# Kernel tuning notes

Measured on AMD Instinct MI355X. Metric: run time of the kernel, lower is better.

Reference implementation:

```python
import jax, jax.numpy as jnp
import numpy as np

B, N, K, D, H = 1, 2048, 32, 128, 8
DH = D // H
EPS = 1e-5


def eq_linear(s, v, Ws, bs, Wv):
    # scalar channels: affine; vector channels: linear only (equivariance)
    return s @ Ws + bs, jnp.einsum('...ix,io->...ox', v, Wv)


def dtp(s1, v1, s2, v2, w=None):
    # depthwise tensor product paths: s*s, v.v (scalars); s1*v2, s2*v1 (vectors)
    ss = s1 * s2
    vv = jnp.sum(v1 * v2, axis=-1)
    sv = s1[..., None] * v2
    vs = s2[..., None] * v1
    if w is not None:  # w: [4, ...] per-path per-channel weights
        ss = ss * w[0]
        vv = vv * w[1]
        sv = sv * w[2][..., None]
        vs = vs * w[3][..., None]
    return jnp.concatenate([ss, vv], -1), jnp.concatenate([sv, vs], -2)


def eq_layer_norm(s, v, gs, bs, gv):
    mu = s.mean(-1, keepdims=True)
    var = ((s - mu) ** 2).mean(-1, keepdims=True)
    s_ln = (s - mu) / jnp.sqrt(var + EPS) * gs + bs
    # vectors: normalize by RMS of channel norms (rotation-equivariant)
    rms = jnp.sqrt(jnp.mean(jnp.sum(v * v, -1), -1, keepdims=True) + EPS)
    v_ln = v / rms[..., None] * gv[..., None]
    return s_ln, v_ln


def layer_norm(x, g, b):
    mu = x.mean(-1, keepdims=True)
    var = ((x - mu) ** 2).mean(-1, keepdims=True)
    return (x - mu) / jnp.sqrt(var + EPS) * g + b


def setup_inputs() -> dict:
    key = jax.random.key(0)
    ks = jax.random.split(key, 32)
    r = lambda i, sh, sc=1.0: jax.random.normal(ks[i], sh, jnp.float32) * sc
    inp = {
        'query_s': r(0, (B, N, D)), 'query_v': r(1, (B, N, D, 3)),
        'key_s': r(2, (B, N, D)), 'key_v': r(3, (B, N, D, 3)),
        'edge_irrep_s': r(4, (B, N, K)), 'edge_irrep_v': r(5, (B, N, K, 3)),
        'edge_emb': r(6, (B, N, K, D)),
        'pair_attn_mask': jnp.logical_or(
            jax.random.randint(ks[7], (B, N, K), 0, 2) > 0, jnp.arange(K) == 0),
        'knn_key_index': jax.random.randint(ks[8], (B, N, K), 0, N),
        # EquivariantLinear params
        'Wq_s': r(9, (D, D), D ** -0.5), 'Wq_v': r(10, (D, D), D ** -0.5), 'bq': jnp.zeros(D),
        'Wk_s': r(11, (D, D), D ** -0.5), 'Wk_v': r(12, (D, D), D ** -0.5), 'bk': jnp.zeros(D),
        'Wqk_s': r(13, (2 * DH, DH), (2 * DH) ** -0.5), 'Wqk_v': r(14, (2 * DH, DH), (2 * DH) ** -0.5), 'bqk': jnp.zeros(DH),
        'Wdtp': r(15, (D, 4 * D), D ** -0.5), 'bdtp': jnp.zeros(4 * D),
        'Wagv_s': r(16, (H, 2 * DH, 3 * DH), (2 * DH) ** -0.5), 'bagv': jnp.zeros((H, 3 * DH)),
        'Wagv_v': r(17, (H, 2 * DH, DH), (2 * DH) ** -0.5),
        'Wattn': r(18, (DH,), DH ** -0.5),
        'Wval_s': r(19, (2 * DH, DH), (2 * DH) ** -0.5), 'Wval_v': r(20, (2 * DH, DH), (2 * DH) ** -0.5), 'bval': jnp.zeros(DH),
        'Wo_s': r(21, (D, D), D ** -0.5), 'Wo_v': r(22, (D, D), D ** -0.5), 'bo': jnp.zeros(D),
        'ln_gs': jnp.ones(D), 'ln_bs': jnp.zeros(D), 'ln_gv': jnp.ones(D),
        'lna_g': jnp.ones(DH), 'lna_b': jnp.zeros(DH),
    }
    return inp


def reference(query_s, query_v, key_s, key_v, edge_irrep_s, edge_irrep_v, edge_emb,
              pair_attn_mask, knn_key_index,
              Wq_s, Wq_v, bq, Wk_s, Wk_v, bk, Wqk_s, Wqk_v, bqk, Wdtp, bdtp,
              Wagv_s, bagv, Wagv_v, Wattn, Wval_s, Wval_v, bval, Wo_s, Wo_v, bo,
              ln_gs, ln_bs, ln_gv, lna_g, lna_b):
    # pre-LN + skip (LAYER_NORM_ON_SKIP=True: skip taken after LN)
    qs, qv = eq_layer_norm(query_s, query_v, ln_gs, ln_bs, ln_gv)
    skip_s, skip_v = qs, qv
    qs, qv = eq_linear(qs, qv, Wq_s, bq, Wq_v)
    ksc, kvc = eq_linear(key_s, key_v, Wk_s, bk, Wk_v)
    # KNN gather of keys per query: [B,Q,K,D] / [B,Q,K,D,3]
    bidx = jnp.arange(B)[:, None, None]
    ks_g = ksc[bidx, knn_key_index]
    kv_g = kvc[bidx, knn_key_index]
    # depthwise tensor product query x gathered keys -> [B,Q,K,2D]
    qk_s, qk_v = dtp(qs[:, :, None, :], qv[:, :, None, :, :], ks_g, kv_g)
    # split heads -> [H,B,Q,K,2DH]
    qk_s = jnp.moveaxis(qk_s.reshape(B, N, K, H, 2 * DH), -2, 0)
    qk_v = jnp.moveaxis(qk_v.reshape(B, N, K, H, 2 * DH, 3), -3, 0)
    qk_s, qk_v = eq_linear(qk_s, qk_v, Wqk_s, bqk, Wqk_v)  # [H,B,Q,K,DH]
    # edge-conditioned TP weights: [4,H,B,Q,K,DH]
    w = (edge_emb @ Wdtp + bdtp).reshape(B, N, K, 4, H, DH)
    w = jnp.transpose(w, (3, 4, 0, 1, 2, 5))
    e_s = edge_irrep_s[..., None]        # [B,Q,K,1]
    e_v = edge_irrep_v[..., None, :]     # [B,Q,K,1,3]
    qk_s, qk_v = dtp(qk_s, qk_v, e_s, e_v, w)  # [H,B,Q,K,2DH]
    # multi-head attn/gate/value projection
    agv = jnp.einsum('hbqki,hio->hbqko', qk_s, Wagv_s) + bagv[:, None, None, None, :]
    val_v = jnp.einsum('hbqkix,hio->hbqkox', qk_v, Wagv_v)  # [H,B,Q,K,DH,3]
    attn_feat, gate, val_s = jnp.split(agv, 3, axis=-1)
    attn = jnp.einsum('hbqkd,d->hbqk', layer_norm(attn_feat, lna_g, lna_b), Wattn)
    attn = jnp.where(pair_attn_mask[None], attn, jnp.finfo(attn.dtype).min)
    attn = jax.nn.softmax(attn, axis=-1)
    # gate activation: SiLU on scalars, sigmoid-gate on vectors
    val_s = jax.nn.silu(val_s)
    val_v = val_v * jax.nn.sigmoid(gate)[..., None]
    # value-edge tensor product + projection
    vs2, vv2 = dtp(val_s, val_v, e_s, e_v)
    vs2, vv2 = eq_linear(vs2, vv2, Wval_s, bval, Wval_v)  # [H,B,Q,K,DH]
    # attention-weighted aggregation over neighbors
    out_s = jnp.einsum('hbqkd,hbqk->hbqd', vs2, attn)
    out_v = jnp.einsum('hbqkdx,hbqk->hbqdx', vv2, attn)
    out_s = jnp.moveaxis(out_s, 0, -2).reshape(B, N, D)
    out_v = jnp.moveaxis(out_v, 0, -3).reshape(B, N, D, 3)
    out_s, out_v = eq_linear(out_s, out_v, Wo_s, bo, Wo_v)
    return out_s + skip_s, out_v + skip_v, attn
```

## Files before the change

### kernel.cpp

```cpp
#include <hip/hip_runtime.h>
#include <hip/hip_bf16.h>
#include <math.h>

#define N_Q 2048
#define K_E 32
#define D_F 128
#define H_N 8
#define DH_N 16
#define EPS_F 1e-5f
#define NEGMAX -3.4028235e38f
#define EPB 8


__global__ __launch_bounds__(64) void k_prep(
    const int* __restrict__ mask, int* __restrict__ kidx, int* __restrict__ ucnt,
    float* __restrict__ attn_raw, float* __restrict__ mbuf)
{
    const int n = blockIdx.x, t = threadIdx.x;
    const int k = t & 31;
    int mk = (t < 32) ? mask[n*K_E + k] : 0;
    unsigned long long bal = __ballot(mk != 0);
    int u = (int)__popcll(bal);
    if (t < 32 && mk) {
        int pos = (int)__popcll(bal & ((1ull << k) - 1ull));
        kidx[n*K_E + pos] = k;
    }
    if (t == 0) ucnt[n] = u;
    if (mask[n*K_E + k] == 0) {
        int hb = (t >> 5) * 4;
        #pragma unroll
        for (int hh = 0; hh < 4; ++hh)
            attn_raw[(size_t)(hb + hh)*(N_Q*K_E) + n*K_E + k] = NEGMAX;
    }
    int gU = (u + 7) >> 3;
    if (t < 16) {
        for (int g2 = gU; g2 < 4; ++g2)
            mbuf[(n*4 + g2)*16 + t] = (t < 8) ? NEGMAX : 0.f;
    }
}

__global__ __launch_bounds__(128) void k_qk(
    const float* __restrict__ qs_in, const float* __restrict__ qv_in,
    const float* __restrict__ ks_in, const float* __restrict__ kv_in,
    const float* __restrict__ Wq_s, const float* __restrict__ Wq_v, const float* __restrict__ bq,
    const float* __restrict__ Wk_s, const float* __restrict__ Wk_v, const float* __restrict__ bk,
    const float* __restrict__ ln_gs, const float* __restrict__ ln_bs, const float* __restrict__ ln_gv,
    float4* __restrict__ q4, float4* __restrict__ k4,
    float* __restrict__ skip_s, float* __restrict__ skip_v)
{
    const int t = threadIdx.x;
    __shared__ __align__(16) float raw[D_F*3];
    __shared__ float4 sv[D_F];
    __shared__ float red[6];
    if (blockIdx.x < N_Q) {
        const int n = blockIdx.x;
        float sval = qs_in[n*D_F + t];
        float ssqp = 0.f;
        if (t < 96) {
            float4 rv = ((const float4*)(qv_in + (size_t)n*D_F*3))[t];
            ((float4*)raw)[t] = rv;
            ssqp = rv.x*rv.x + rv.y*rv.y + rv.z*rv.z + rv.w*rv.w;
        }
        float r0 = sval, r1 = sval*sval, r2 = ssqp;
        #pragma unroll
        for (int m = 1; m < 64; m <<= 1) {
            r0 += __shfl_xor(r0, m);
            r1 += __shfl_xor(r1, m);
            r2 += __shfl_xor(r2, m);
        }
        if ((t & 63) == 0) { int w = t >> 6; red[w*3+0]=r0; red[w*3+1]=r1; red[w*3+2]=r2; }
        __syncthreads();
        float tS = red[0]+red[3], tS2 = red[1]+red[4], tQ = red[2]+red[5];
        float mu = tS * (1.f/D_F);
        float var = fmaxf(tS2*(1.f/D_F) - mu*mu, 0.f);
        float rstd = rsqrtf(var + EPS_F);
        float rrms = rsqrtf(tQ*(1.f/D_F) + EPS_F);
        float a = (sval - mu)*rstd*ln_gs[t] + ln_bs[t];
        skip_s[n*D_F + t] = a;
        float gv = ln_gv[t];
        float b0 = raw[t*3+0]*rrms*gv;
        float b1 = raw[t*3+1]*rrms*gv;
        float b2 = raw[t*3+2]*rrms*gv;
        skip_v[(n*D_F + t)*3 + 0] = b0;
        skip_v[(n*D_F + t)*3 + 1] = b1;
        skip_v[(n*D_F + t)*3 + 2] = b2;
        sv[t] = make_float4(b0, b1, b2, a);
        __syncthreads();
        float acc = bq[t], a0 = 0.f, a1 = 0.f, a2 = 0.f;
        #pragma unroll 4
        for (int i = 0; i < D_F; ++i) {
            float4 p = sv[i];
            float ws = Wq_s[i*D_F + t];
            float wv = Wq_v[i*D_F + t];
            acc += p.w*ws; a0 += p.x*wv; a1 += p.y*wv; a2 += p.z*wv;
        }
        q4[n*D_F + t] = make_float4(a0, a1, a2, acc);
    } else {
        const int n = blockIdx.x - N_Q;
        float sval = ks_in[n*D_F + t];
        if (t < 96) ((float4*)raw)[t] = ((const float4*)(kv_in + (size_t)n*D_F*3))[t];
        __syncthreads();
        sv[t] = make_float4(raw[t*3+0], raw[t*3+1], raw[t*3+2], sval);
        __syncthreads();
        float acc = bk[t], a0 = 0.f, a1 = 0.f, a2 = 0.f;
        #pragma unroll 4
        for (int i = 0; i < D_F; ++i) {
            float4 p = sv[i];
            float ws = Wk_s[i*D_F + t];
            float wv = Wk_v[i*D_F + t];
            acc += p.w*ws; a0 += p.x*wv; a1 += p.y*wv; a2 += p.z*wv;
        }
        k4[n*D_F + t] = make_float4(a0, a1, a2, acc);
    }
}

__global__ __launch_bounds__(512, 6) void k_edge_flash(
    const float4* __restrict__ q4, const float4* __restrict__ k4,
    const float* __restrict__ eis, const float* __restrict__ eiv,
    const float* __restrict__ eemb,
    const int* __restrict__ knn,
    const int* __restrict__ kidx, const int* __restrict__ ucnt,
    const float* __restrict__ Wqk_s, const float* __restrict__ Wqk_v, const float* __restrict__ bqk,
    const float* __restrict__ Wdtp, const float* __restrict__ bdtp,
    const float* __restrict__ Wagv_s, const float* __restrict__ bagv, const float* __restrict__ Wagv_v,
    const float* __restrict__ Wattn, const float* __restrict__ lna_g, const float* __restrict__ lna_b,
    const float* __restrict__ Wval_s, const float* __restrict__ Wval_v, const float* __restrict__ bval,
    float4* __restrict__ pbuf, float* __restrict__ mbuf, float* __restrict__ attn_raw)
{
    const int n = blockIdx.x & (N_Q - 1);
    const int g = blockIdx.x >> 11;
    const int base = n*K_E;
    const int u = ucnt[n];
    if ((g << 3) >= u) return;

    const int t = threadIdx.x;
    const int s = t >> 7, c = t & 127, h = (t >> 4) & 7, o = t & 15;
    const int rot2 = h * 2;

    __shared__ float4 ch[EPB*256];
    __shared__ float4 w4[EPB*128];
    __shared__ float  afeat[EPB*8*17];
    __shared__ float  mred[16];

    {
        float* ee = (float*)ch;
        {
            int idx = t; int m = idx & 7, i = idx >> 3;
            int jj = (g<<3) + m; jj = (jj < u) ? jj : (u-1);
            int e = base + kidx[base + jj];
            ee[i*EPB+m] = eemb[(size_t)e*D_F + i];
        }
        {
            int idx = t + 512; int m = idx & 7, i = idx >> 3;
            int jj = (g<<3) + m; jj = (jj < u) ? jj : (u-1);
            int e = base + kidx[base + jj];
            ee[i*EPB+m] = eemb[(size_t)e*D_F + i];
        }
        __syncthreads();
        float acc[EPB];
        float b = bdtp[t];
        #pragma unroll
        for (int m = 0; m < EPB; ++m) acc[m] = b;
        #pragma unroll 2
        for (int i = 0; i < D_F; ++i) {
            float wv = Wdtp[i*512 + t];
            #pragma unroll
            for (int m = 0; m < EPB; ++m) acc[m] += ee[i*EPB+m]*wv;
        }
        __syncthreads();
        float* w4f = (float*)w4;
        const int chn = t & 127, sel = t >> 7;
        #pragma unroll
        for (int m = 0; m < EPB; ++m)
            w4f[(m*128 + chn)*4 + sel] = acc[m];
    }

    const int mA = s, mB = s + 4;
    int jA = (g<<3) + mA; jA = (jA < u) ? jA : (u-1);
    int jB = (g<<3) + mB; jB = (jB < u) ? jB : (u-1);
    const int eA = base + kidx[base + jA];
    const int eB = base + kidx[base + jB];

    const float esA = eis[eA], esB = eis[eB];
    const float evAx = eiv[eA*3+0], evAy = eiv[eA*3+1], evAz = eiv[eA*3+2];
    const float evBx = eiv[eB*3+0], evBy = eiv[eB*3+1], evBz = eiv[eB*3+2];

    {
        float4 q  = q4[(size_t)n*D_F + c];
        float4 kA = k4[(size_t)knn[eA]*D_F + c];
        float4 kB = k4[(size_t)knn[eB]*D_F + c];
        const int hp = c >> 5, jc = c & 31;
        const int pos0 = hp*32 + ((jc + 2*hp) & 31);
        const int pos1 = (hp+4)*32 + ((jc + 2*(hp+4)) & 31);
        ch[mA*256 + pos0] = make_float4(q.w*kA.x, q.w*kA.y, q.w*kA.z, q.w*kA.w);
        ch[mA*256 + pos1] = make_float4(kA.w*q.x, kA.w*q.y, kA.w*q.z,
                                        q.x*kA.x + q.y*kA.y + q.z*kA.z);
        ch[mB*256 + pos0] = make_float4(q.w*kB.x, q.w*kB.y, q.w*kB.z, q.w*kB.w);
        ch[mB*256 + pos1] = make_float4(kB.w*q.x, kB.w*q.y, kB.w*q.z,
                                        q.x*kB.x + q.y*kB.y + q.z*kB.z);
    }
    __syncthreads();

    const int chA = mA*256 + h*32, chB = mB*256 + h*32;

    float pAs, pA0, pA1, pA2, pBs, pB0, pB1, pB2;
    {
        const float bqk_r = bqk[o];
        pAs = bqk_r; pA0 = 0.f; pA1 = 0.f; pA2 = 0.f;
        pBs = bqk_r; pB0 = 0.f; pB1 = 0.f; pB2 = 0.f;
        #pragma unroll 4
        for (int i = 0; i < 32; ++i) {
            int ph = (i + rot2) & 31;
            float4 cA = ch[chA + ph];
            float4 cB = ch[chB + ph];
            float ws = Wqk_s[i*16 + o];
            float wv = Wqk_v[i*16 + o];
            pAs += cA.w*ws; pA0 += cA.x*wv; pA1 += cA.y*wv; pA2 += cA.z*wv;
            pBs += cB.w*ws; pB0 += cB.x*wv; pB1 += cB.y*wv; pB2 += cB.z*wv;
        }
    }
    __syncthreads();

    const int posA = h*32 + ((o + rot2) & 31);
    const int posB = h*32 + ((o + 16 + rot2) & 31);

    {
        float4 wA = w4[mA*128 + c];
        float4 wB = w4[mB*128 + c];
        ch[mA*256 + posA] = make_float4(pAs*evAx*wA.z, pAs*evAy*wA.z, pAs*evAz*wA.z, pAs*esA*wA.x);
        float dA = pA0*evAx + pA1*evAy + pA2*evAz;
        ch[mA*256 + posB] = make_float4(esA*pA0*wA.w, esA*pA1*wA.w, esA*pA2*wA.w, dA*wA.y);
        ch[mB*256 + posA] = make_float4(pBs*evBx*wB.z, pBs*evBy*wB.z, pBs*evBz*wB.z, pBs*esB*wB.x);
        float dB = pB0*evBx + pB1*evBy + pB2*evBz;
        ch[mB*256 + posB] = make_float4(esB*pB0*wB.w, esB*pB1*wB.w, esB*pB2*wB.w, dB*wB.y);
    }
    __syncthreads();

    float gtA, vlA, vA0, vA1, vA2, gtB, vlB, vB0, vB1, vB2;
    {
        const float bag0 = bagv[h*48 + o];
        const float bag1 = bagv[h*48 + 16 + o];
        const float bag2 = bagv[h*48 + 32 + o];
        float atA = bag0, atB = bag0;
        gtA = bag1; vlA = bag2; vA0 = 0.f; vA1 = 0.f; vA2 = 0.f;
        gtB = bag1; vlB = bag2; vB0 = 0.f; vB1 = 0.f; vB2 = 0.f;
        #pragma unroll 4
        for (int i = 0; i < 32; ++i) {
            int ph = (i + rot2) & 31;
            float4 cA = ch[chA + ph];
            float4 cB = ch[chB + ph];
            const float* wrow = &Wagv_s[(h*32+i)*48];
            float w0 = wrow[o], w1 = wrow[16+o], w2 = wrow[32+o];
            float wv = Wagv_v[(h*32+i)*16 + o];
            atA += cA.w*w0; gtA += cA.w*w1; vlA += cA.w*w2;
            vA0 += cA.x*wv; vA1 += cA.y*wv; vA2 += cA.z*wv;
            atB += cB.w*w0; gtB += cB.w*w1; vlB += cB.w*w2;
            vB0 += cB.x*wv; vB1 += cB.y*wv; vB2 += cB.z*wv;
        }
        afeat[(mA*8 + h)*17 + o] = atA;
        afeat[(mB*8 + h)*17 + o] = atB;
    }
    __syncthreads();

    if (t < EPB*H_N) {
        int m2 = t >> 3, h2 = t & 7;
        const float* afr = &afeat[(m2*8 + h2)*17];
        float mu = 0.f;
        #pragma unroll 4
        for (int d2 = 0; d2 < DH_N; ++d2) mu += afr[d2];
        mu *= (1.f/DH_N);
        float var = 0.f;
        #pragma unroll 4
        for (int d2 = 0; d2 < DH_N; ++d2) { float dd = afr[d2]-mu; var += dd*dd; }
        var *= (1.f/DH_N);
        float rstd = rsqrtf(var + EPS_F);
        float logit = 0.f;
        #pragma unroll 4
        for (int d2 = 0; d2 < DH_N; ++d2) {
            float xn = (afr[d2]-mu)*rstd*lna_g[d2] + lna_b[d2];
            logit += xn*Wattn[d2];
        }
        int jj = (g<<3) + m2;
        bool vok = jj < u;
        if (vok) {
            int kor = kidx[base + jj];
            attn_raw[h2*(N_Q*K_E) + n*K_E + kor] = logit;
        } else {
            logit = NEGMAX;
        }
        afeat[(m2*8 + h2)*17 + 16] = logit;
        float mx = logit;
        mx = fmaxf(mx, __shfl_xor(mx, 8));
        mx = fmaxf(mx, __shfl_xor(mx, 16));
        mx = fmaxf(mx, __shfl_xor(mx, 32));
        float ex = expf(logit - mx);
        ex += __shfl_xor(ex, 8);
        ex += __shfl_xor(ex, 16);
        ex += __shfl_xor(ex, 32);
        if (m2 == 0) { mred[h2] = mx; mred[8 + h2] = ex; }
    }
    float sactA = vlA / (1.f + expf(-vlA));
    float gA = 1.f / (1.f + expf(-gtA));
    float qA0 = vA0*gA, qA1 = vA1*gA, qA2 = vA2*gA;
    float sactB = vlB / (1.f + expf(-vlB));
    float gB = 1.f / (1.f + expf(-gtB));
    float qB0 = vB0*gB, qB1 = vB1*gB, qB2 = vB2*gB;

    {
        ch[mA*256 + posA] = make_float4(sactA*evAx, sactA*evAy, sactA*evAz, sactA*esA);
        float dA = qA0*evAx + qA1*evAy + qA2*evAz;
        ch[mA*256 + posB] = make_float4(esA*qA0, esA*qA1, esA*qA2, dA);
        ch[mB*256 + posA] = make_float4(sactB*evBx, sactB*evBy, sactB*evBz, sactB*esB);
        float dB = qB0*evBx + qB1*evBy + qB2*evBz;
        ch[mB*256 + posB] = make_float4(esB*qB0, esB*qB1, esB*qB2, dB);
    }
    __syncthreads();

    {
        const float bval_r = bval[o];
        float vsA = bval_r, uA0 = 0.f, uA1 = 0.f, uA2 = 0.f;
        float vsB = bval_r, uB0 = 0.f, uB1 = 0.f, uB2 = 0.f;
        #pragma unroll 4
        for (int i = 0; i < 32; ++i) {
            int ph = (i + rot2) & 31;
            float4 cA = ch[chA + ph];
            float4 cB = ch[chB + ph];
            float ws = Wval_s[i*16 + o];
            float wv = Wval_v[i*16 + o];
            vsA += cA.w*ws; uA0 += cA.x*wv; uA1 += cA.y*wv; uA2 += cA.z*wv;
            vsB += cB.w*ws; uB0 += cB.x*wv; uB1 += cB.y*wv; uB2 += cB.z*wv;
        }
        float lA = afeat[(mA*8 + h)*17 + 16];
        float lB = afeat[(mB*8 + h)*17 + 16];
        float Mg = mred[h];
        float wgA = expf(lA - Mg);
        float wgB = expf(lB - Mg);
        w4[s*128 + c] = make_float4(wgA*uA0 + wgB*uB0, wgA*uA1 + wgB*uB1,
                                    wgA*uA2 + wgB*uB2, wgA*vsA + wgB*vsB);
    }
    __syncthreads();

    if (t < 128) {
        float4 a = w4[t], b4 = w4[128 + t], c4 = w4[256 + t], d4 = w4[384 + t];
        pbuf[((size_t)(n*4 + g))*D_F + t] =
            make_float4(a.x + b4.x + c4.x + d4.x, a.y + b4.y + c4.y + d4.y,
                        a.z + b4.z + c4.z + d4.z, a.w + b4.w + c4.w + d4.w);
    } else if (t < 144) {
        mbuf[(n*4 + g)*16 + (t - 128)] = mred[t - 128];
    }
}

__global__ __launch_bounds__(128) void k_finish(
    const float4* __restrict__ pbuf, const float* __restrict__ mbuf,
    float* __restrict__ attn_out,
    const float* __restrict__ skip_s, const float* __restrict__ skip_v,
    const float* __restrict__ Wo_s, const float* __restrict__ Wo_v, const float* __restrict__ bo,
    float* __restrict__ out0, float* __restrict__ out1)
{
    const int n = blockIdx.x, t = threadIdx.x;
    __shared__ float Ms[H_N], Dn[H_N];
    __shared__ float4 xsh[D_F];
    if (t < 32) {
        int h3 = t >> 2, g3 = t & 3;
        float mg = mbuf[(n*4 + g3)*16 + h3];
        float dg = mbuf[(n*4 + g3)*16 + 8 + h3];
        float mx = mg;
        mx = fmaxf(mx, __shfl_xor(mx, 1));
        mx = fmaxf(mx, __shfl_xor(mx, 2));
        float dsc = dg * expf(mg - mx);
        dsc += __shfl_xor(dsc, 1);
        dsc += __shfl_xor(dsc, 2);
        if (g3 == 0) { Ms[h3] = mx; Dn[h3] = dsc; }
    }
    __syncthreads();
    const int h = t >> 4, o = t & 15;
    const float M = Ms[h];
    const float rden = 1.f / Dn[h];
    float4 acc = make_float4(0.f, 0.f, 0.f, 0.f);
    #pragma unroll
    for (int gg = 0; gg < 4; ++gg) {
        float mg = mbuf[(n*4 + gg)*16 + h];
        if (mg > -1e37f) {
            float4 pv = pbuf[((size_t)(n*4 + gg))*D_F + t];
            float sf = expf(mg - M) * rden;
            acc.x += pv.x*sf; acc.y += pv.y*sf; acc.z += pv.z*sf; acc.w += pv.w*sf;
        }
    }
    xsh[t] = acc;
    #pragma unroll
    for (int kk = 0; kk < 2; ++kk) {
        size_t idx = (size_t)h*(N_Q*K_E) + (size_t)n*K_E + (o + kk*16);
        attn_out[idx] = expf(attn_out[idx] - M) * rden;
    }
    __syncthreads();
    float acc_s = bo[t], o0 = 0.f, o1 = 0.f, o2 = 0.f;
    #pragma unroll 4
    for (int i = 0; i < D_F; ++i) {
        float4 x = xsh[i];
        float ws = Wo_s[i*D_F + t];
        float wv = Wo_v[i*D_F + t];
        acc_s += x.w*ws; o0 += x.x*wv; o1 += x.y*wv; o2 += x.z*wv;
    }
    out0[n*D_F + t] = acc_s + skip_s[n*D_F + t];
    out1[(n*D_F + t)*3 + 0] = o0 + skip_v[(n*D_F + t)*3 + 0];
    out1[(n*D_F + t)*3 + 1] = o1 + skip_v[(n*D_F + t)*3 + 1];
    out1[(n*D_F + t)*3 + 2] = o2 + skip_v[(n*D_F + t)*3 + 2];
}

extern "C" void kernel_launch(void* const* d_in, const int* in_sizes, int n_in,
                              void* d_out, int out_size, void* d_ws, size_t ws_size,
                              hipStream_t stream)
{
    (void)in_sizes; (void)n_in; (void)out_size; (void)ws_size;

    const float* query_s = (const float*)d_in[0];
    const float* query_v = (const float*)d_in[1];
    const float* key_s   = (const float*)d_in[2];
    const float* key_v   = (const float*)d_in[3];
    const float* eis     = (const float*)d_in[4];
    const float* eiv     = (const float*)d_in[5];
    const float* eemb    = (const float*)d_in[6];
    const int*   mask    = (const int*)d_in[7];
    const int*   knn     = (const int*)d_in[8];
    const float* Wq_s    = (const float*)d_in[9];
    const float* Wq_v    = (const float*)d_in[10];
    const float* bq      = (const float*)d_in[11];
    const float* Wk_s    = (const float*)d_in[12];
    const float* Wk_v    = (const float*)d_in[13];
    const float* bk      = (const float*)d_in[14];
    const float* Wqk_s   = (const float*)d_in[15];
    const float* Wqk_v   = (const float*)d_in[16];
    const float* bqk     = (const float*)d_in[17];
    const float* Wdtp    = (const float*)d_in[18];
    const float* bdtp    = (const float*)d_in[19];
    const float* Wagv_s  = (const float*)d_in[20];
    const float* bagv    = (const float*)d_in[21];
    const float* Wagv_v  = (const float*)d_in[22];
    const float* Wattn   = (const float*)d_in[23];
    const float* Wval_s  = (const float*)d_in[24];
    const float* Wval_v  = (const float*)d_in[25];
    const float* bval    = (const float*)d_in[26];
    const float* Wo_s    = (const float*)d_in[27];
    const float* Wo_v    = (const float*)d_in[28];
    const float* bo      = (const float*)d_in[29];
    const float* ln_gs   = (const float*)d_in[30];
    const float* ln_bs   = (const float*)d_in[31];
    const float* ln_gv   = (const float*)d_in[32];
    const float* lna_g   = (const float*)d_in[33];
    const float* lna_b   = (const float*)d_in[34];

    float* out      = (float*)d_out;
    float* out_s    = out;
    float* out_v    = out + N_Q*D_F;
    float* out_attn = out + N_Q*D_F*4;

    float* ws = (float*)d_ws;
    float4* q4     = (float4*)ws;
    float4* k4     = q4 + N_Q*D_F;
    float*  skip_s = (float*)(k4 + N_Q*D_F);
    float*  skip_v = skip_s + N_Q*D_F;
    float4* pbuf   = (float4*)(skip_v + N_Q*D_F*3);
    float*  mbuf   = (float*)(pbuf + N_Q*4*D_F);
    int*    kidx   = (int*)(mbuf + N_Q*4*16);
    int*    ucnt   = kidx + N_Q*K_E;

    hipLaunchKernelGGL(k_prep, dim3(N_Q), dim3(64), 0, stream,
                       mask, kidx, ucnt, out_attn, mbuf);
    hipLaunchKernelGGL(k_qk, dim3(2*N_Q), dim3(D_F), 0, stream,
                       query_s, query_v, key_s, key_v,
                       Wq_s, Wq_v, bq, Wk_s, Wk_v, bk,
                       ln_gs, ln_bs, ln_gv,
                       q4, k4, skip_s, skip_v);
    hipLaunchKernelGGL(k_edge_flash, dim3(N_Q*K_E/EPB), dim3(512), 0, stream,
                       q4, k4, eis, eiv, eemb, knn, kidx, ucnt,
                       Wqk_s, Wqk_v, bqk, Wdtp, bdtp,
                       Wagv_s, bagv, Wagv_v, Wattn, lna_g, lna_b,
                       Wval_s, Wval_v, bval,
                       pbuf, mbuf, out_attn);
    hipLaunchKernelGGL(k_finish, dim3(N_Q), dim3(D_F), 0, stream,
                       pbuf, mbuf, out_attn, skip_s, skip_v, Wo_s, Wo_v, bo,
                       out_s, out_v);
}
```

Before: 436.4 us.

## Fuse mask prep into k_qk and pre-pack edge weights into interleaved vectors

```diff
diff --git a/kernel.cpp b/kernel.cpp
--- a/kernel.cpp
+++ b/kernel.cpp
@@ -12,41 +12,21 @@
 #define EPB 8
 
 
-__global__ __launch_bounds__(64) void k_prep(
-    const int* __restrict__ mask, int* __restrict__ kidx, int* __restrict__ ucnt,
-    float* __restrict__ attn_raw, float* __restrict__ mbuf)
-{
-    const int n = blockIdx.x, t = threadIdx.x;
-    const int k = t & 31;
-    int mk = (t < 32) ? mask[n*K_E + k] : 0;
-    unsigned long long bal = __ballot(mk != 0);
-    int u = (int)__popcll(bal);
-    if (t < 32 && mk) {
-        int pos = (int)__popcll(bal & ((1ull << k) - 1ull));
-        kidx[n*K_E + pos] = k;
-    }
-    if (t == 0) ucnt[n] = u;
-    if (mask[n*K_E + k] == 0) {
-        int hb = (t >> 5) * 4;
-        #pragma unroll
-        for (int hh = 0; hh < 4; ++hh)
-            attn_raw[(size_t)(hb + hh)*(N_Q*K_E) + n*K_E + k] = NEGMAX;
-    }
-    int gU = (u + 7) >> 3;
-    if (t < 16) {
-        for (int g2 = gU; g2 < 4; ++g2)
-            mbuf[(n*4 + g2)*16 + t] = (t < 8) ? NEGMAX : 0.f;
-    }
-}
-
 __global__ __launch_bounds__(128) void k_qk(
     const float* __restrict__ qs_in, const float* __restrict__ qv_in,
     const float* __restrict__ ks_in, const float* __restrict__ kv_in,
     const float* __restrict__ Wq_s, const float* __restrict__ Wq_v, const float* __restrict__ bq,
     const float* __restrict__ Wk_s, const float* __restrict__ Wk_v, const float* __restrict__ bk,
     const float* __restrict__ ln_gs, const float* __restrict__ ln_bs, const float* __restrict__ ln_gv,
+    const int* __restrict__ mask,
+    const float* __restrict__ Wqk_s, const float* __restrict__ Wqk_v,
+    const float* __restrict__ Wagv_s, const float* __restrict__ Wagv_v,
+    const float* __restrict__ Wval_s, const float* __restrict__ Wval_v,
     float4* __restrict__ q4, float4* __restrict__ k4,
-    float* __restrict__ skip_s, float* __restrict__ skip_v)
+    float* __restrict__ skip_s, float* __restrict__ skip_v,
+    int* __restrict__ kidx, int* __restrict__ ucnt,
+    float* __restrict__ attn_raw, float* __restrict__ mbuf,
+    float* __restrict__ wpk)
 {
     const int t = threadIdx.x;
     __shared__ __align__(16) float raw[D_F*3];
@@ -54,6 +34,28 @@
     __shared__ float red[6];
     if (blockIdx.x < N_Q) {
         const int n = blockIdx.x;
+        if (t < 64) {
+            const int k = t & 31;
+            int mk = (t < 32) ? mask[n*K_E + k] : 0;
+            unsigned long long bal = __ballot(mk != 0);
+            int u = (int)__popcll(bal);
+            if (t < 32 && mk) {
+                int pos = (int)__popcll(bal & ((1ull << k) - 1ull));
+                kidx[n*K_E + pos] = k;
+            }
+            if (t == 0) ucnt[n] = u;
+            if (mask[n*K_E + k] == 0) {
+                int hb = (t >> 5) * 4;
+                #pragma unroll
+                for (int hh = 0; hh < 4; ++hh)
+                    attn_raw[(size_t)(hb + hh)*(N_Q*K_E) + n*K_E + k] = NEGMAX;
+            }
+            int gU = (u + 7) >> 3;
+            if (t < 16) {
+                for (int g2 = gU; g2 < 4; ++g2)
+                    mbuf[(n*4 + g2)*16 + t] = (t < 8) ? NEGMAX : 0.f;
+            }
+        }
         float sval = qs_in[n*D_F + t];
         float ssqp = 0.f;
         if (t < 96) {
@@ -97,6 +99,22 @@
         q4[n*D_F + t] = make_float4(a0, a1, a2, acc);
     } else {
         const int n = blockIdx.x - N_Q;
+        if (n < 288 && t < 64) {
+            int pid = n*64 + t;
+            float v;
+            if (pid < 1024) {
+                int p = pid >> 1, comp = pid & 1;
+                v = comp ? Wqk_v[p] : Wqk_s[p];
+            } else if (pid < 17408) {
+                int x = pid - 1024; int e = x >> 2, comp = x & 3;
+                int row = e >> 4, o = e & 15;
+                v = (comp < 3) ? Wagv_s[row*48 + comp*16 + o] : Wagv_v[row*16 + o];
+            } else {
+                int x = pid - 17408; int p = x >> 1, comp = x & 1;
+                v = comp ? Wval_v[p] : Wval_s[p];
+            }
+            wpk[pid] = v;
+        }
         float sval = ks_in[n*D_F + t];
         if (t < 96) ((float4*)raw)[t] = ((const float4*)(kv_in + (size_t)n*D_F*3))[t];
         __syncthreads();
@@ -120,11 +138,11 @@
     const float* __restrict__ eemb,
     const int* __restrict__ knn,
     const int* __restrict__ kidx, const int* __restrict__ ucnt,
-    const float* __restrict__ Wqk_s, const float* __restrict__ Wqk_v, const float* __restrict__ bqk,
+    const float* __restrict__ wpk, const float* __restrict__ bqk,
     const float* __restrict__ Wdtp, const float* __restrict__ bdtp,
-    const float* __restrict__ Wagv_s, const float* __restrict__ bagv, const float* __restrict__ Wagv_v,
+    const float* __restrict__ bagv,
     const float* __restrict__ Wattn, const float* __restrict__ lna_g, const float* __restrict__ lna_b,
-    const float* __restrict__ Wval_s, const float* __restrict__ Wval_v, const float* __restrict__ bval,
+    const float* __restrict__ bval,
     float4* __restrict__ pbuf, float* __restrict__ mbuf, float* __restrict__ attn_raw)
 {
     const int n = blockIdx.x & (N_Q - 1);
@@ -136,6 +154,10 @@
     const int t = threadIdx.x;
     const int s = t >> 7, c = t & 127, h = (t >> 4) & 7, o = t & 15;
     const int rot2 = h * 2;
+
+    const float2* wqk  = (const float2*)wpk;
+    const float4* wag  = (const float4*)(wpk + 1024);
+    const float2* wvl  = (const float2*)(wpk + 17408);
 
     __shared__ float4 ch[EPB*256];
     __shared__ float4 w4[EPB*128];
@@ -213,10 +235,9 @@
             int ph = (i + rot2) & 31;
             float4 cA = ch[chA + ph];
             float4 cB = ch[chB + ph];
-            float ws = Wqk_s[i*16 + o];
-            float wv = Wqk_v[i*16 + o];
-            pAs += cA.w*ws; pA0 += cA.x*wv; pA1 += cA.y*wv; pA2 += cA.z*wv;
-            pBs += cB.w*ws; pB0 += cB.x*wv; pB1 += cB.y*wv; pB2 += cB.z*wv;
+            float2 w = wqk[i*16 + o];
+            pAs += cA.w*w.x; pA0 += cA.x*w.y; pA1 += cA.y*w.y; pA2 += cA.z*w.y;
+            pBs += cB.w*w.x; pB0 += cB.x*w.y; pB1 += cB.y*w.y; pB2 += cB.z*w.y;
         }
     }
     __syncthreads();
@@ -249,13 +270,11 @@
             int ph = (i + rot2) & 31;
             float4 cA = ch[chA + ph];
             float4 cB = ch[chB + ph];
-            const float* wrow = &Wagv_s[(h*32+i)*48];
-            float w0 = wrow[o], w1 = wrow[16+o], w2 = wrow[32+o];
-            float wv = Wagv_v[(h*32+i)*16 + o];
-            atA += cA.w*w0; gtA += cA.w*w1; vlA += cA.w*w2;
-            vA0 += cA.x*wv; vA1 += cA.y*wv; vA2 += cA.z*wv;
-            atB += cB.w*w0; gtB += cB.w*w1; vlB += cB.w*w2;
-            vB0 += cB.x*wv; vB1 += cB.y*wv; vB2 += cB.z*wv;
+            float4 wg = wag[(h*32+i)*16 + o];
+            atA += cA.w*wg.x; gtA += cA.w*wg.y; vlA += cA.w*wg.z;
+            vA0 += cA.x*wg.w; vA1 += cA.y*wg.w; vA2 += cA.z*wg.w;
+            atB += cB.w*wg.x; gtB += cB.w*wg.y; vlB += cB.w*wg.z;
+            vB0 += cB.x*wg.w; vB1 += cB.y*wg.w; vB2 += cB.z*wg.w;
         }
         afeat[(mA*8 + h)*17 + o] = atA;
         afeat[(mB*8 + h)*17 + o] = atB;
@@ -325,10 +344,9 @@
             int ph = (i + rot2) & 31;
             float4 cA = ch[chA + ph];
             float4 cB = ch[chB + ph];
-            float ws = Wval_s[i*16 + o];
-            float wv = Wval_v[i*16 + o];
-            vsA += cA.w*ws; uA0 += cA.x*wv; uA1 += cA.y*wv; uA2 += cA.z*wv;
-            vsB += cB.w*ws; uB0 += cB.x*wv; uB1 += cB.y*wv; uB2 += cB.z*wv;
+            float2 w = wvl[i*16 + o];
+            vsA += cA.w*w.x; uA0 += cA.x*w.y; uA1 += cA.y*w.y; uA2 += cA.z*w.y;
+            vsB += cB.w*w.x; uB0 += cB.x*w.y; uB1 += cB.y*w.y; uB2 += cB.z*w.y;
         }
         float lA = afeat[(mA*8 + h)*17 + 16];
         float lB = afeat[(mB*8 + h)*17 + 16];
@@ -463,19 +481,19 @@
     float*  mbuf   = (float*)(pbuf + N_Q*4*D_F);
     int*    kidx   = (int*)(mbuf + N_Q*4*16);
     int*    ucnt   = kidx + N_Q*K_E;
-
-    hipLaunchKernelGGL(k_prep, dim3(N_Q), dim3(64), 0, stream,
-                       mask, kidx, ucnt, out_attn, mbuf);
+    float*  wpk    = (float*)(ucnt + N_Q);
+
     hipLaunchKernelGGL(k_qk, dim3(2*N_Q), dim3(D_F), 0, stream,
                        query_s, query_v, key_s, key_v,
                        Wq_s, Wq_v, bq, Wk_s, Wk_v, bk,
                        ln_gs, ln_bs, ln_gv,
-                       q4, k4, skip_s, skip_v);
+                       mask, Wqk_s, Wqk_v, Wagv_s, Wagv_v, Wval_s, Wval_v,
+                       q4, k4, skip_s, skip_v,
+                       kidx, ucnt, out_attn, mbuf, wpk);
     hipLaunchKernelGGL(k_edge_flash, dim3(N_Q*K_E/EPB), dim3(512), 0, stream,
                        q4, k4, eis, eiv, eemb, knn, kidx, ucnt,
-                       Wqk_s, Wqk_v, bqk, Wdtp, bdtp,
-                       Wagv_s, bagv, Wagv_v, Wattn, lna_g, lna_b,
-                       Wval_s, Wval_v, bval,
+                       wpk, bqk, Wdtp, bdtp,
+                       bagv, Wattn, lna_g, lna_b, bval,
                        pbuf, mbuf, out_attn);
     hipLaunchKernelGGL(k_finish, dim3(N_Q), dim3(D_F), 0, stream,
                        pbuf, mbuf, out_attn, skip_s, skip_v, Wo_s, Wo_v, bo,
```

After: 446.1 us. 2.2% more time.

## Fuse prep into qk kernel and finish into edge kernel via last-block atomic

Applied to the files above, without the earlier changes.

```diff
diff --git a/kernel.cpp b/kernel.cpp
--- a/kernel.cpp
+++ b/kernel.cpp
@@ -12,41 +12,17 @@
 #define EPB 8
 
 
-__global__ __launch_bounds__(64) void k_prep(
-    const int* __restrict__ mask, int* __restrict__ kidx, int* __restrict__ ucnt,
-    float* __restrict__ attn_raw, float* __restrict__ mbuf)
-{
-    const int n = blockIdx.x, t = threadIdx.x;
-    const int k = t & 31;
-    int mk = (t < 32) ? mask[n*K_E + k] : 0;
-    unsigned long long bal = __ballot(mk != 0);
-    int u = (int)__popcll(bal);
-    if (t < 32 && mk) {
-        int pos = (int)__popcll(bal & ((1ull << k) - 1ull));
-        kidx[n*K_E + pos] = k;
-    }
-    if (t == 0) ucnt[n] = u;
-    if (mask[n*K_E + k] == 0) {
-        int hb = (t >> 5) * 4;
-        #pragma unroll
-        for (int hh = 0; hh < 4; ++hh)
-            attn_raw[(size_t)(hb + hh)*(N_Q*K_E) + n*K_E + k] = NEGMAX;
-    }
-    int gU = (u + 7) >> 3;
-    if (t < 16) {
-        for (int g2 = gU; g2 < 4; ++g2)
-            mbuf[(n*4 + g2)*16 + t] = (t < 8) ? NEGMAX : 0.f;
-    }
-}
-
 __global__ __launch_bounds__(128) void k_qk(
     const float* __restrict__ qs_in, const float* __restrict__ qv_in,
     const float* __restrict__ ks_in, const float* __restrict__ kv_in,
     const float* __restrict__ Wq_s, const float* __restrict__ Wq_v, const float* __restrict__ bq,
     const float* __restrict__ Wk_s, const float* __restrict__ Wk_v, const float* __restrict__ bk,
     const float* __restrict__ ln_gs, const float* __restrict__ ln_bs, const float* __restrict__ ln_gv,
+    const int* __restrict__ mask,
     float4* __restrict__ q4, float4* __restrict__ k4,
-    float* __restrict__ skip_s, float* __restrict__ skip_v)
+    float* __restrict__ skip_s, float* __restrict__ skip_v,
+    int* __restrict__ kidx, int* __restrict__ ucnt, int* __restrict__ cnt,
+    float* __restrict__ attn_raw, float* __restrict__ mbuf)
 {
     const int t = threadIdx.x;
     __shared__ __align__(16) float raw[D_F*3];
@@ -54,6 +30,28 @@
     __shared__ float red[6];
     if (blockIdx.x < N_Q) {
         const int n = blockIdx.x;
+        if (t < 64) {
+            const int k = t & 31;
+            int mk = (t < 32) ? mask[n*K_E + k] : 0;
+            unsigned long long bal = __ballot(mk != 0);
+            int u = (int)__popcll(bal);
+            if (t < 32 && mk) {
+                int pos = (int)__popcll(bal & ((1ull << k) - 1ull));
+                kidx[n*K_E + pos] = k;
+            }
+            if (t == 0) { ucnt[n] = u; cnt[n] = 0; }
+            if (mask[n*K_E + k] == 0) {
+                int hb = (t >> 5) * 4;
+                #pragma unroll
+                for (int hh = 0; hh < 4; ++hh)
+                    attn_raw[(size_t)(hb + hh)*(N_Q*K_E) + n*K_E + k] = NEGMAX;
+            }
+            int gU = (u + 7) >> 3;
+            if (t < 16) {
+                for (int g2 = gU; g2 < 4; ++g2)
+                    mbuf[(n*4 + g2)*16 + t] = (t < 8) ? NEGMAX : 0.f;
+            }
+        }
         float sval = qs_in[n*D_F + t];
         float ssqp = 0.f;
         if (t < 96) {
@@ -119,13 +117,16 @@
     const float* __restrict__ eis, const float* __restrict__ eiv,
     const float* __restrict__ eemb,
     const int* __restrict__ knn,
-    const int* __restrict__ kidx, const int* __restrict__ ucnt,
+    const int* __restrict__ kidx, const int* __restrict__ ucnt, int* __restrict__ cnt,
     const float* __restrict__ Wqk_s, const float* __restrict__ Wqk_v, const float* __restrict__ bqk,
     const float* __restrict__ Wdtp, const float* __restrict__ bdtp,
     const float* __restrict__ Wagv_s, const float* __restrict__ bagv, const float* __restrict__ Wagv_v,
     const float* __restrict__ Wattn, const float* __restrict__ lna_g, const float* __restrict__ lna_b,
     const float* __restrict__ Wval_s, const float* __restrict__ Wval_v, const float* __restrict__ bval,
-    float4* __restrict__ pbuf, float* __restrict__ mbuf, float* __restrict__ attn_raw)
+    const float* __restrict__ Wo_s, const float* __restrict__ Wo_v, const float* __restrict__ bo,
+    const float* __restrict__ skip_s, const float* __restrict__ skip_v,
+    float4* __restrict__ pbuf, float* __restrict__ mbuf, float* __restrict__ attn_raw,
+    float* __restrict__ out0, float* __restrict__ out1)
 {
     const int n = blockIdx.x & (N_Q - 1);
     const int g = blockIdx.x >> 11;
@@ -141,6 +142,8 @@
     __shared__ float4 w4[EPB*128];
     __shared__ float  afeat[EPB*8*17];
     __shared__ float  mred[16];
+    __shared__ float  MsDn[16];
+    __shared__ int    lastFlag;
 
     {
         float* ee = (float*)ch;
@@ -348,18 +351,19 @@
     } else if (t < 144) {
         mbuf[(n*4 + g)*16 + (t - 128)] = mred[t - 128];
     }
-}
-
-__global__ __launch_bounds__(128) void k_finish(
-    const float4* __restrict__ pbuf, const float* __restrict__ mbuf,
-    float* __restrict__ attn_out,
-    const float* __restrict__ skip_s, const float* __restrict__ skip_v,
-    const float* __restrict__ Wo_s, const float* __restrict__ Wo_v, const float* __restrict__ bo,
-    float* __restrict__ out0, float* __restrict__ out1)
-{
-    const int n = blockIdx.x, t = threadIdx.x;
-    __shared__ float Ms[H_N], Dn[H_N];
-    __shared__ float4 xsh[D_F];
+    __syncthreads();
+
+    if (t == 0) {
+        __threadfence();
+        int nact = (u + 7) >> 3;
+        int old = atomicAdd(&cnt[n], 1);
+        int last = (old == nact - 1);
+        if (last) __threadfence();
+        lastFlag = last;
+    }
+    __syncthreads();
+    if (!lastFlag) return;
+
     if (t < 32) {
         int h3 = t >> 2, g3 = t & 3;
         float mg = mbuf[(n*4 + g3)*16 + h3];
@@ -370,41 +374,56 @@
         float dsc = dg * expf(mg - mx);
         dsc += __shfl_xor(dsc, 1);
         dsc += __shfl_xor(dsc, 2);
-        if (g3 == 0) { Ms[h3] = mx; Dn[h3] = dsc; }
-    }
-    __syncthreads();
-    const int h = t >> 4, o = t & 15;
-    const float M = Ms[h];
-    const float rden = 1.f / Dn[h];
-    float4 acc = make_float4(0.f, 0.f, 0.f, 0.f);
-    #pragma unroll
-    for (int gg = 0; gg < 4; ++gg) {
-        float mg = mbuf[(n*4 + gg)*16 + h];
-        if (mg > -1e37f) {
-            float4 pv = pbuf[((size_t)(n*4 + gg))*D_F + t];
-            float sf = expf(mg - M) * rden;
-            acc.x += pv.x*sf; acc.y += pv.y*sf; acc.z += pv.z*sf; acc.w += pv.w*sf;
-        }
-    }
-    xsh[t] = acc;
-    #pragma unroll
-    for (int kk = 0; kk < 2; ++kk) {
-        size_t idx = (size_t)h*(N_Q*K_E) + (size_t)n*K_E + (o + kk*16);
-        attn_out[idx] = expf(attn_out[idx] - M) * rden;
-    }
-    __syncthreads();
-    float acc_s = bo[t], o0 = 0.f, o1 = 0.f, o2 = 0.f;
-    #pragma unroll 4
-    for (int i = 0; i < D_F; ++i) {
-        float4 x = xsh[i];
-        float ws = Wo_s[i*D_F + t];
-        float wv = Wo_v[i*D_F + t];
-        acc_s += x.w*ws; o0 += x.x*wv; o1 += x.y*wv; o2 += x.z*wv;
-    }
-    out0[n*D_F + t] = acc_s + skip_s[n*D_F + t];
-    out1[(n*D_F + t)*3 + 0] = o0 + skip_v[(n*D_F + t)*3 + 0];
-    out1[(n*D_F + t)*3 + 1] = o1 + skip_v[(n*D_F + t)*3 + 1];
-    out1[(n*D_F + t)*3 + 2] = o2 + skip_v[(n*D_F + t)*3 + 2];
+        if (g3 == 0) { MsDn[h3] = mx; MsDn[8 + h3] = dsc; }
+    }
+    __syncthreads();
+    if (t < 128) {
+        int hh = t >> 4, oo = t & 15;
+        const float M = MsDn[hh];
+        const float rden = 1.f / MsDn[8 + hh];
+        float4 a4 = make_float4(0.f, 0.f, 0.f, 0.f);
+        #pragma unroll
+        for (int gg = 0; gg < 4; ++gg) {
+            float mg = mbuf[(n*4 + gg)*16 + hh];
+            if (mg > -1e37f) {
+                float4 pv = pbuf[((size_t)(n*4 + gg))*D_F + t];
+                float sf = expf(mg - M) * rden;
+                a4.x += pv.x*sf; a4.y += pv.y*sf; a4.z += pv.z*sf; a4.w += pv.w*sf;
+            }
+        }
+        ch[1024 + t] = a4;
+        #pragma unroll
+        for (int kk = 0; kk < 2; ++kk) {
+            size_t idx = (size_t)hh*(N_Q*K_E) + (size_t)n*K_E + (oo + kk*16);
+            attn_raw[idx] = expf(attn_raw[idx] - M) * rden;
+        }
+    }
+    __syncthreads();
+    {
+        float po_s = 0.f, po0 = 0.f, po1 = 0.f, po2 = 0.f;
+        const int ib = s*32;
+        #pragma unroll 4
+        for (int ii = 0; ii < 32; ++ii) {
+            int i = ib + ii;
+            float4 x = ch[1024 + i];
+            float ws = Wo_s[i*D_F + c];
+            float wv = Wo_v[i*D_F + c];
+            po_s += x.w*ws; po0 += x.x*wv; po1 += x.y*wv; po2 += x.z*wv;
+        }
+        w4[s*128 + c] = make_float4(po0, po1, po2, po_s);
+    }
+    __syncthreads();
+    if (t < 128) {
+        float4 a = w4[t], b4 = w4[128 + t], c4 = w4[256 + t], d4 = w4[384 + t];
+        float os = a.w + b4.w + c4.w + d4.w + bo[t];
+        float o0 = a.x + b4.x + c4.x + d4.x;
+        float o1 = a.y + b4.y + c4.y + d4.y;
+        float o2 = a.z + b4.z + c4.z + d4.z;
+        out0[n*D_F + t] = os + skip_s[n*D_F + t];
+        out1[(n*D_F + t)*3 + 0] = o0 + skip_v[(n*D_F + t)*3 + 0];
+        out1[(n*D_F + t)*3 + 1] = o1 + skip_v[(n*D_F + t)*3 + 1];
+        out1[(n*D_F + t)*3 + 2] = o2 + skip_v[(n*D_F + t)*3 + 2];
+    }
 }
 
 extern "C" void kernel_launch(void* const* d_in, const int* in_sizes, int n_in,
@@ -463,21 +482,19 @@
     float*  mbuf   = (float*)(pbuf + N_Q*4*D_F);
     int*    kidx   = (int*)(mbuf + N_Q*4*16);
     int*    ucnt   = kidx + N_Q*K_E;
-
-    hipLaunchKernelGGL(k_prep, dim3(N_Q), dim3(64), 0, stream,
-                       mask, kidx, ucnt, out_attn, mbuf);
+    int*    cnt    = ucnt + N_Q;
+
     hipLaunchKernelGGL(k_qk, dim3(2*N_Q), dim3(D_F), 0, stream,
                        query_s, query_v, key_s, key_v,
                        Wq_s, Wq_v, bq, Wk_s, Wk_v, bk,
-                       ln_gs, ln_bs, ln_gv,
-                       q4, k4, skip_s, skip_v);
+                       ln_gs, ln_bs, ln_gv, mask,
+                       q4, k4, skip_s, skip_v,
+                       kidx, ucnt, cnt, out_attn, mbuf);
     hipLaunchKernelGGL(k_edge_flash, dim3(N_Q*K_E/EPB), dim3(512), 0, stream,
-                       q4, k4, eis, eiv, eemb, knn, kidx, ucnt,
+                       q4, k4, eis, eiv, eemb, knn, kidx, ucnt, cnt,
                        Wqk_s, Wqk_v, bqk, Wdtp, bdtp,
                        Wagv_s, bagv, Wagv_v, Wattn, lna_g, lna_b,
                        Wval_s, Wval_v, bval,
-                       pbuf, mbuf, out_attn);
-    hipLaunchKernelGGL(k_finish, dim3(N_Q), dim3(D_F), 0, stream,
-                       pbuf, mbuf, out_attn, skip_s, skip_v, Wo_s, Wo_v, bo,
-                       out_s, out_v);
+                       Wo_s, Wo_v, bo, skip_s, skip_v,
+                       pbuf, mbuf, out_attn, out_s, out_v);
 }
```

Result: slower. 553.4 us (+26.8%).
